# Kernel tuning notes

Hardware: AMD Instinct MI355X
Metric: run time of the kernel (lower is better)

The kernel has to match this reference:

```python
import jax, jax.numpy as jnp
import numpy as np

N0, N1, N2 = 100000, 25000, 5000
E0, E1 = 400000, 80000
IN_FEATS, N_HIDDEN, N_CLASSES = 512, 512, 64


def setup_inputs() -> dict:
    key = jax.random.key(0)
    ks = jax.random.split(key, 16)
    return {
        "feats": jax.random.normal(ks[0], (N0, IN_FEATS), jnp.float32),
        "h0_hist": jax.random.normal(ks[1], (N0, N_HIDDEN), jnp.float32),
        "agg_h0": jax.random.normal(ks[2], (N1, N_HIDDEN), jnp.float32),
        "h1_hist": jax.random.normal(ks[3], (N1, 2 * N_HIDDEN), jnp.float32),
        "agg_h1": jax.random.normal(ks[4], (N2, 2 * N_HIDDEN), jnp.float32),
        "W0": jax.random.normal(ks[5], (N_HIDDEN, IN_FEATS), jnp.float32) * 0.02,
        "b0": jax.random.normal(ks[6], (N_HIDDEN,), jnp.float32) * 0.02,
        "W1": jax.random.normal(ks[7], (N_HIDDEN, N_HIDDEN), jnp.float32) * 0.02,
        "b1": jax.random.normal(ks[8], (N_HIDDEN,), jnp.float32) * 0.02,
        "W2": jax.random.normal(ks[9], (N_CLASSES, 2 * N_HIDDEN), jnp.float32) * 0.02,
        "b2": jax.random.normal(ks[10], (N_CLASSES,), jnp.float32) * 0.02,
        "src0": jax.random.randint(ks[11], (E0,), 0, N0, jnp.int64),
        "dst0": jax.random.randint(ks[12], (E0,), 0, N1, jnp.int64),
        "src1": jax.random.randint(ks[13], (E1,), 0, N1, jnp.int64),
        "dst1": jax.random.randint(ks[14], (E1,), 0, N2, jnp.int64),
    }


def _segment_mean(h_src, src, dst, num_dst):
    # copy_src gather + variable-degree mean reduction (DGL fn.mean)
    msg = h_src[src]  # [E, D]
    sums = jax.ops.segment_sum(msg, dst, num_segments=num_dst)
    deg = jax.ops.segment_sum(jnp.ones((src.shape[0],), h_src.dtype), dst,
                              num_segments=num_dst)
    return sums / jnp.maximum(deg, 1.0)[:, None]


def reference(feats, h0_hist, agg_h0, h1_hist, agg_h1,
              W0, b0, W1, b1, W2, b2,
              src0, dst0, src1, dst1):
    # input layer: linear + relu (dropout=0)
    h = jax.nn.relu(feats @ W0.T + b0)  # [N0, H]

    # block 0: control-variate subtract, mean-aggregate, NodeUpdate(1) concat
    h = h - h0_hist
    agg = _segment_mean(h, src0, dst0, agg_h0.shape[0])  # [N1, H]
    h = (agg + agg_h0) @ W1.T + b1
    h = jnp.concatenate([h, jax.nn.relu(h)], axis=1)  # [N1, 2H]

    # block 1: control-variate subtract, mean-aggregate, NodeUpdate(2)
    h = h - h1_hist
    agg = _segment_mean(h, src1, dst1, agg_h1.shape[0])  # [N2, 2H]
    h = (agg + agg_h1) @ W2.T + b2  # [N2, C]
    return h
```

## Files before the change

kernel.cpp:

```cpp
#include <hip/hip_runtime.h>

#define N0c 100000
#define N1c 25000
#define N2c 5000
#define E0c 400000
#define E1c 80000

typedef __attribute__((ext_vector_type(8))) short bf16x8;
typedef __attribute__((ext_vector_type(4))) float f32x4;

#define GLOAD_LDS(g, l) \
    __builtin_amdgcn_global_load_lds((__attribute__((address_space(1))) const unsigned int*)(const void*)(g), \
                                     (__attribute__((address_space(3))) unsigned int*)(void*)(l), 16, 0, 0)

static __device__ __forceinline__ uint rnd_bf(float f) {
    uint u = __float_as_uint(f);
    return (u + 0x7FFFu + ((u >> 16) & 1u)) & 0xFFFF0000u;
}
static __device__ __forceinline__ unsigned short to_bf(float f) {
    return (unsigned short)(rnd_bf(f) >> 16);
}
static __device__ __forceinline__ uint pk_bf(float f0, float f1) {
    return (rnd_bf(f0) >> 16) | rnd_bf(f1);
}

__global__ __launch_bounds__(256)
void presplit_bf(const float* __restrict__ X, uint4* __restrict__ out,
                 int M, int tile0, int ntiles)
{
    const int id = blockIdx.x * 256 + threadIdx.x;
    const int slot = id & 1023;
    const int tk = id >> 10;
    if (tk >= ntiles * 8) return;
    const int kt8 = tk & 7, mtl = tk >> 3;
    const int r = slot >> 3, p = slot & 7;
    const int o = p ^ (r & 7);
    const int row = (tile0 + mtl) * 128 + r;
    uint4 v = {0u, 0u, 0u, 0u};
    if (row < M) {
        const float* src = X + (size_t)row * 512 + kt8 * 64 + o * 8;
        float4 x0 = *(const float4*)src;
        float4 x1 = *(const float4*)(src + 4);
        v.x = pk_bf(x0.x, x0.y); v.y = pk_bf(x0.z, x0.w);
        v.z = pk_bf(x1.x, x1.y); v.w = pk_bf(x1.z, x1.w);
    }
    out[(size_t)tk * 1024 + slot] = v;
}

template<int EPI>
__global__ __launch_bounds__(256, 2)
void gemm_bf16(const uint4* __restrict__ At, const uint4* __restrict__ Bt,
               const float* __restrict__ bias, const float* __restrict__ hist,
               unsigned short* __restrict__ C, int Mreal, int row_off, int nblk)
{
    __shared__ uint4 lds[2048];

    const int tid = threadIdx.x;
    const int orig = blockIdx.x;
    const int xcd = orig & 7, q = nblk >> 3, rr = nblk & 7;
    const int lid = (xcd < rr ? xcd * (q + 1) : rr * (q + 1) + (xcd - rr) * q) + (orig >> 3);
    const int bm = lid >> 2, bn = lid & 3;

    const int w = tid >> 6, lane = tid & 63;
    const int wm = w >> 1, wn = w & 1;
    const int lg = lane >> 4, lr = lane & 15;
    const int sw = lr & 7;
    const int sbase = w * 256;

    const uint4* Abase = At + (size_t)bm * 8 * 1024;
    const uint4* Bbase = Bt + (size_t)bn * 8 * 1024;

    f32x4 acc[4][4];
#pragma unroll
    for (int i = 0; i < 4; ++i)
#pragma unroll
        for (int j = 0; j < 4; ++j) acc[i][j] = {0.f, 0.f, 0.f, 0.f};

    for (int kt = 0; kt < 8; ++kt) {
        if (kt) __syncthreads();
        const uint4* Atile = Abase + (size_t)kt * 1024;
        const uint4* Btile = Bbase + (size_t)kt * 1024;
#pragma unroll
        for (int j = 0; j < 4; ++j) {
            const int slot = sbase + j * 64 + lane;
            GLOAD_LDS(Atile + slot, &lds[slot]);
            GLOAD_LDS(Btile + slot, &lds[1024 + slot]);
        }
        __syncthreads();

        bf16x8 a[4][2], b[4][2];
#pragma unroll
        for (int mi = 0; mi < 4; ++mi) {
            const uint4* rp = &lds[(wm * 64 + mi * 16 + lr) * 8];
            a[mi][0] = *(const bf16x8*)&rp[lg ^ sw];
            a[mi][1] = *(const bf16x8*)&rp[(4 + lg) ^ sw];
        }
#pragma unroll
        for (int ni = 0; ni < 4; ++ni) {
            const uint4* rp = &lds[1024 + (wn * 64 + ni * 16 + lr) * 8];
            b[ni][0] = *(const bf16x8*)&rp[lg ^ sw];
            b[ni][1] = *(const bf16x8*)&rp[(4 + lg) ^ sw];
        }
#pragma unroll
        for (int kk = 0; kk < 2; ++kk)
#pragma unroll
            for (int mi = 0; mi < 4; ++mi)
#pragma unroll
                for (int ni = 0; ni < 4; ++ni)
                    acc[mi][ni] = __builtin_amdgcn_mfma_f32_16x16x32_bf16(
                        a[mi][kk], b[ni][kk], acc[mi][ni], 0, 0, 0);
    }

#pragma unroll
    for (int mi = 0; mi < 4; ++mi)
#pragma unroll
        for (int ni = 0; ni < 4; ++ni) {
            const int col = bn * 128 + wn * 64 + ni * 16 + lr;
            const float bv = bias[col];
#pragma unroll
            for (int r = 0; r < 4; ++r) {
                const int m = row_off + bm * 128 + wm * 64 + mi * 16 + lg * 4 + r;
                if (m < Mreal) {
                    const float v = acc[mi][ni][r] + bv;
                    if (EPI == 0) {
                        C[(size_t)m * 512 + col] = to_bf(fmaxf(v, 0.f) - hist[(size_t)m * 512 + col]);
                    } else {
                        C[(size_t)m * 1024 + col]       = to_bf(v - hist[(size_t)m * 1024 + col]);
                        C[(size_t)m * 1024 + 512 + col] = to_bf(fmaxf(v, 0.f) - hist[(size_t)m * 1024 + 512 + col]);
                    }
                }
            }
        }
}

__global__ __launch_bounds__(256)
void gemm64(const float* __restrict__ A, const float* __restrict__ B,
            const float* __restrict__ bias, float* __restrict__ C, int M)
{
    const int K = 1024;
    __shared__ float As[32][68];
    __shared__ float Bs[32][68];
    const int tid = threadIdx.x;
    const int tx = tid & 15, ty = tid >> 4;
    const int lrow = tid >> 3;
    const int lk   = (tid & 7) * 4;
    const int bm = blockIdx.x;

    float acc[4][4];
#pragma unroll
    for (int i = 0; i < 4; ++i)
#pragma unroll
        for (int j = 0; j < 4; ++j) acc[i][j] = 0.f;

    int ar0 = bm * 64 + lrow;      if (ar0 > M - 1) ar0 = M - 1;
    int ar1 = bm * 64 + 32 + lrow; if (ar1 > M - 1) ar1 = M - 1;

    for (int kt = 0; kt < K; kt += 32) {
        float4 a0 = *(const float4*)(A + (size_t)ar0 * K + kt + lk);
        float4 a1 = *(const float4*)(A + (size_t)ar1 * K + kt + lk);
        float4 b0 = *(const float4*)(B + (size_t)lrow * K + kt + lk);
        float4 b1 = *(const float4*)(B + (size_t)(32 + lrow) * K + kt + lk);
        __syncthreads();
        As[lk+0][lrow]    = a0.x; As[lk+1][lrow]    = a0.y; As[lk+2][lrow]    = a0.z; As[lk+3][lrow]    = a0.w;
        As[lk+0][lrow+32] = a1.x; As[lk+1][lrow+32] = a1.y; As[lk+2][lrow+32] = a1.z; As[lk+3][lrow+32] = a1.w;
        Bs[lk+0][lrow]    = b0.x; Bs[lk+1][lrow]    = b0.y; Bs[lk+2][lrow]    = b0.z; Bs[lk+3][lrow]    = b0.w;
        Bs[lk+0][lrow+32] = b1.x; Bs[lk+1][lrow+32] = b1.y; Bs[lk+2][lrow+32] = b1.z; Bs[lk+3][lrow+32] = b1.w;
        __syncthreads();
#pragma unroll
        for (int kk = 0; kk < 32; ++kk) {
            float4 av = *(const float4*)&As[kk][ty * 4];
            float4 bv = *(const float4*)&Bs[kk][tx * 4];
            float aa[4] = {av.x, av.y, av.z, av.w};
            float bb[4] = {bv.x, bv.y, bv.z, bv.w};
#pragma unroll
            for (int i = 0; i < 4; ++i)
#pragma unroll
                for (int j = 0; j < 4; ++j)
                    acc[i][j] += aa[i] * bb[j];
        }
    }

    const float4 bv = *(const float4*)&bias[tx * 4];
#pragma unroll
    for (int i = 0; i < 4; ++i) {
        const int m = bm * 64 + ty * 4 + i;
        if (m >= M) continue;
        float4 o;
        o.x = acc[i][0] + bv.x; o.y = acc[i][1] + bv.y;
        o.z = acc[i][2] + bv.z; o.w = acc[i][3] + bv.w;
        *(float4*)&C[(size_t)m * 64 + tx * 4] = o;
    }
}

__global__ void count_deg(const int* __restrict__ dst, int* __restrict__ deg, int E)
{
    int e = blockIdx.x * blockDim.x + threadIdx.x;
    if (e < E) atomicAdd(&deg[dst[e]], 1);
}

__global__ __launch_bounds__(1024)
void exscan(const int* __restrict__ deg, int* __restrict__ off, int* __restrict__ cur, int n)
{
    __shared__ int wsum[16];
    __shared__ int carry;
    const int tid = threadIdx.x, lane = tid & 63, w = tid >> 6;
    if (tid == 0) carry = 0;
    __syncthreads();
    for (int base = 0; base < n; base += 1024) {
        const int i = base + tid;
        const int v = (i < n) ? deg[i] : 0;
        int x = v;
#pragma unroll
        for (int d = 1; d < 64; d <<= 1) {
            int y = __shfl_up(x, d, 64);
            if (lane >= d) x += y;
        }
        if (lane == 63) wsum[w] = x;
        __syncthreads();
        int wo = 0, tot = 0;
#pragma unroll
        for (int k = 0; k < 16; ++k) { int s = wsum[k]; tot += s; if (k < w) wo += s; }
        const int excl = carry + wo + x - v;
        if (i < n) { off[i] = excl; cur[i] = excl; }
        __syncthreads();
        if (tid == 0) carry += tot;
        __syncthreads();
    }
    if (tid == 0) off[n] = carry;
}

__global__ void scatter_edges(const int* __restrict__ src, const int* __restrict__ dst,
                              int* __restrict__ cur, int* __restrict__ eidx, int E)
{
    int e = blockIdx.x * blockDim.x + threadIdx.x;
    if (e < E) {
        int p = atomicAdd(&cur[dst[e]], 1);
        eidx[p] = src[e];
    }
}

__global__ __launch_bounds__(256)
void seg_mean_split(const unsigned short* __restrict__ h, const int* __restrict__ off,
                    const int* __restrict__ eidx, const float* __restrict__ addin,
                    uint4* __restrict__ out, int n_dst, int n_pad)
{
    const int wid = blockIdx.x * 4 + (threadIdx.x >> 6);
    const int lane = threadIdx.x & 63;
    if (wid >= n_pad) return;
    uint4 v = {0u, 0u, 0u, 0u};
    if (wid < n_dst) {
        const int e0 = off[wid], e1 = off[wid + 1];
        float s[8];
#pragma unroll
        for (int i = 0; i < 8; ++i) s[i] = 0.f;
        for (int e = e0; e < e1; ++e) {
            const uint4 vv = *((const uint4*)(h + (size_t)eidx[e] * 512) + lane);
            const uint u[4] = {vv.x, vv.y, vv.z, vv.w};
#pragma unroll
            for (int i = 0; i < 4; ++i) {
                s[2 * i]     += __uint_as_float(u[i] << 16);
                s[2 * i + 1] += __uint_as_float(u[i] & 0xFFFF0000u);
            }
        }
        const float sc = 1.0f / (float)((e1 - e0) > 0 ? (e1 - e0) : 1);
        const float* ad = addin + (size_t)wid * 512 + lane * 8;
        float4 d0 = *(const float4*)ad;
        float4 d1 = *(const float4*)(ad + 4);
        v.x = pk_bf(s[0] * sc + d0.x, s[1] * sc + d0.y);
        v.y = pk_bf(s[2] * sc + d0.z, s[3] * sc + d0.w);
        v.z = pk_bf(s[4] * sc + d1.x, s[5] * sc + d1.y);
        v.w = pk_bf(s[6] * sc + d1.z, s[7] * sc + d1.w);
    }
    const int mt = wid >> 7, r = wid & 127;
    const int kt8 = lane >> 3, o = lane & 7;
    out[((size_t)(mt * 8 + kt8)) * 1024 + r * 8 + (o ^ (r & 7))] = v;
}

__global__ __launch_bounds__(256)
void seg_mean_add4(const unsigned short* __restrict__ h, const int* __restrict__ off,
                   const int* __restrict__ eidx, const float* __restrict__ addin,
                   float* __restrict__ out, int n_dst)
{
    const int wid = blockIdx.x * 4 + (threadIdx.x >> 6);
    const int lane = threadIdx.x & 63;
    if (wid >= n_dst) return;
    const int e0 = off[wid], e1 = off[wid + 1];
    float s[16];
#pragma unroll
    for (int i = 0; i < 16; ++i) s[i] = 0.f;
    for (int e = e0; e < e1; ++e) {
        const uint4* row = (const uint4*)(h + (size_t)eidx[e] * 1024);
#pragma unroll
        for (int half = 0; half < 2; ++half) {
            const uint4 v = row[lane + 64 * half];
            const uint u[4] = {v.x, v.y, v.z, v.w};
#pragma unroll
            for (int i = 0; i < 4; ++i) {
                s[8 * half + 2 * i]     += __uint_as_float(u[i] << 16);
                s[8 * half + 2 * i + 1] += __uint_as_float(u[i] & 0xFFFF0000u);
            }
        }
    }
    const float sc = 1.0f / (float)((e1 - e0) > 0 ? (e1 - e0) : 1);
#pragma unroll
    for (int half = 0; half < 2; ++half) {
        const float* ad = addin + (size_t)wid * 1024 + half * 512 + lane * 8;
        float* o = out + (size_t)wid * 1024 + half * 512 + lane * 8;
        float4 d0 = *(const float4*)ad;
        float4 d1 = *(const float4*)(ad + 4);
        float4 r0, r1;
        r0.x = s[8*half+0] * sc + d0.x; r0.y = s[8*half+1] * sc + d0.y;
        r0.z = s[8*half+2] * sc + d0.z; r0.w = s[8*half+3] * sc + d0.w;
        r1.x = s[8*half+4] * sc + d1.x; r1.y = s[8*half+5] * sc + d1.y;
        r1.z = s[8*half+6] * sc + d1.z; r1.w = s[8*half+7] * sc + d1.w;
        *(float4*)o = r0;
        *(float4*)(o + 4) = r1;
    }
}

extern "C" void kernel_launch(void* const* d_in, const int* in_sizes, int n_in,
                              void* d_out, int out_size, void* d_ws, size_t ws_size,
                              hipStream_t stream)
{
    const float* feats   = (const float*)d_in[0];
    const float* h0_hist = (const float*)d_in[1];
    const float* agg_h0  = (const float*)d_in[2];
    const float* h1_hist = (const float*)d_in[3];
    const float* agg_h1  = (const float*)d_in[4];
    const float* W0 = (const float*)d_in[5];
    const float* b0 = (const float*)d_in[6];
    const float* W1 = (const float*)d_in[7];
    const float* b1 = (const float*)d_in[8];
    const float* W2 = (const float*)d_in[9];
    const float* b2 = (const float*)d_in[10];
    const int* src0 = (const int*)d_in[11];
    const int* dst0 = (const int*)d_in[12];
    const int* src1 = (const int*)d_in[13];
    const int* dst1 = (const int*)d_in[14];

    const int MT1 = 782;
    const int MT2 = 196;
    const size_t TILEB = 8 * 1024 * 16;

    const size_t h0B   = ((size_t)N0c * 512 * 2 + 255) & ~(size_t)255;
    const size_t a2B   = (size_t)MT2 * TILEB;
    const size_t agg1B = (size_t)N2c * 1024 * 4;
    const size_t wsB   = 4 * 8 * 1024 * 16;
    const size_t intB  = ((size_t)(N1c + (N1c + 1) + N1c + E0c + N2c + (N2c + 1) + N2c + E1c) * 4 + 255) & ~(size_t)255;
    const size_t FIXED = h0B + a2B + agg1B + 2 * wsB + intB;

    size_t avail = (ws_size > FIXED) ? (ws_size - FIXED) : 0;
    int ct = (int)(avail / TILEB);
    if (ct < 8) ct = 8;
    if (ct > MT1) ct = MT1;
    const int nchunks = (MT1 + ct - 1) / ct;

    char* ws = (char*)d_ws;
    uint4* Achunk = (uint4*)ws;                              ws += (size_t)ct * TILEB;
    unsigned short* h0 = (unsigned short*)ws;
    unsigned short* h1cat = h0;                              ws += h0B;
    uint4* A2s    = (uint4*)ws;                              ws += a2B;
    float* agg1   = (float*)ws;                              ws += agg1B;
    uint4* Ws0    = (uint4*)ws;                              ws += wsB;
    uint4* Ws1    = (uint4*)ws;                              ws += wsB;
    int* deg0  = (int*)ws;  ws += sizeof(int) * N1c;
    int* off0  = (int*)ws;  ws += sizeof(int) * (N1c + 1);
    int* cur0  = (int*)ws;  ws += sizeof(int) * N1c;
    int* eidx0 = (int*)ws;  ws += sizeof(int) * E0c;
    int* deg1  = (int*)ws;  ws += sizeof(int) * N2c;
    int* off1  = (int*)ws;  ws += sizeof(int) * (N2c + 1);
    int* cur1  = (int*)ws;  ws += sizeof(int) * N2c;
    int* eidx1 = (int*)ws;

    hipMemsetAsync(deg0, 0, sizeof(int) * N1c, stream);
    hipMemsetAsync(deg1, 0, sizeof(int) * N2c, stream);

    presplit_bf<<<4 * 32, 256, 0, stream>>>(W0, Ws0, 512, 0, 4);
    presplit_bf<<<4 * 32, 256, 0, stream>>>(W1, Ws1, 512, 0, 4);
    count_deg<<<(E0c + 255) / 256, 256, 0, stream>>>(dst0, deg0, E0c);
    exscan<<<1, 1024, 0, stream>>>(deg0, off0, cur0, N1c);
    scatter_edges<<<(E0c + 255) / 256, 256, 0, stream>>>(src0, dst0, cur0, eidx0, E0c);

    for (int c = 0; c < nchunks; ++c) {
        const int t0 = c * ct;
        const int nt = (MT1 - t0 < ct) ? (MT1 - t0) : ct;
        presplit_bf<<<nt * 32, 256, 0, stream>>>(feats, Achunk, N0c, t0, nt);
        const int nblk = nt * 4;
        gemm_bf16<0><<<nblk, 256, 0, stream>>>(Achunk, Ws0, b0, h0_hist, h0, N0c, t0 * 128, nblk);
    }

    seg_mean_split<<<(MT2 * 128) / 4, 256, 0, stream>>>(h0, off0, eidx0, agg_h0, A2s, N1c, MT2 * 128);

    count_deg<<<(E1c + 255) / 256, 256, 0, stream>>>(dst1, deg1, E1c);
    exscan<<<1, 1024, 0, stream>>>(deg1, off1, cur1, N2c);
    scatter_edges<<<(E1c + 255) / 256, 256, 0, stream>>>(src1, dst1, cur1, eidx1, E1c);

    gemm_bf16<1><<<MT2 * 4, 256, 0, stream>>>(A2s, Ws1, b1, h1_hist, h1cat, N1c, 0, MT2 * 4);

    seg_mean_add4<<<(N2c + 3) / 4, 256, 0, stream>>>(h1cat, off1, eidx1, agg_h1, agg1, N2c);

    gemm64<<<(N2c + 63) / 64, 256, 0, stream>>>(agg1, W2, b2, (float*)d_out, N2c);
}
```

Before: 592.1 us.

## Fuse fp32-to-bf16 conversion into a row-resident GEMM with double-buffered weights

Replaces the chunked presplit-then-GEMM flow with one kernel per layer. Each block keeps a full 128x512 A row-tile in LDS, converting fp32 feats to bf16 directly on load for layer 0, then loops over all four N tiles while double-buffering W slices. This removes the intermediate bf16 copy of feats (a large write plus re-read) and the repeated A loads across N tiles. In exchange it uses about 160KB of LDS for one block per CU, and the A tile load does not overlap with compute.

```diff
diff --git a/kernel.cpp b/kernel.cpp
--- a/kernel.cpp
+++ b/kernel.cpp
@@ -47,28 +47,56 @@
     out[(size_t)tk * 1024 + slot] = v;
 }
 
-template<int EPI>
-__global__ __launch_bounds__(256, 2)
-void gemm_bf16(const uint4* __restrict__ At, const uint4* __restrict__ Bt,
-               const float* __restrict__ bias, const float* __restrict__ hist,
-               unsigned short* __restrict__ C, int Mreal, int row_off, int nblk)
-{
-    __shared__ uint4 lds[2048];
+template<int SRC, int EPI>
+__global__ __launch_bounds__(256, 1)
+void gemm_persist(const float* __restrict__ Af32, const uint4* __restrict__ At,
+                  const uint4* __restrict__ Bt, const float* __restrict__ bias,
+                  const float* __restrict__ hist, unsigned short* __restrict__ C,
+                  int Mreal, int nblk)
+{
+    __shared__ uint4 lds[10240];
 
     const int tid = threadIdx.x;
     const int orig = blockIdx.x;
     const int xcd = orig & 7, q = nblk >> 3, rr = nblk & 7;
-    const int lid = (xcd < rr ? xcd * (q + 1) : rr * (q + 1) + (xcd - rr) * q) + (orig >> 3);
-    const int bm = lid >> 2, bn = lid & 3;
+    const int bm = (xcd < rr ? xcd * (q + 1) : rr * (q + 1) + (xcd - rr) * q) + (orig >> 3);
 
     const int w = tid >> 6, lane = tid & 63;
     const int wm = w >> 1, wn = w & 1;
     const int lg = lane >> 4, lr = lane & 15;
     const int sw = lr & 7;
-    const int sbase = w * 256;
-
-    const uint4* Abase = At + (size_t)bm * 8 * 1024;
-    const uint4* Bbase = Bt + (size_t)bn * 8 * 1024;
+
+    if (SRC == 0) {
+        const int r = tid >> 1, half = tid & 1;
+        int g = bm * 128 + r; if (g > Mreal - 1) g = Mreal - 1;
+        const float* Arow = Af32 + (size_t)g * 512 + half * 256;
+        const int abase = r * 8;
+        const int rsw = r & 7;
+#pragma unroll 8
+        for (int i = 0; i < 32; ++i) {
+            float4 x0 = *(const float4*)(Arow + i * 8);
+            float4 x1 = *(const float4*)(Arow + i * 8 + 4);
+            uint4 v;
+            v.x = pk_bf(x0.x, x0.y); v.y = pk_bf(x0.z, x0.w);
+            v.z = pk_bf(x1.x, x1.y); v.w = pk_bf(x1.z, x1.w);
+            const int kt = half * 4 + (i >> 3), o = i & 7;
+            lds[kt * 1024 + abase + (o ^ rsw)] = v;
+        }
+    } else {
+        const uint4* Ablk = At + (size_t)bm * 8192;
+#pragma unroll
+        for (int j = 0; j < 32; ++j) {
+            const int slot = w * 2048 + j * 64 + lane;
+            GLOAD_LDS(Ablk + slot, &lds[slot]);
+        }
+    }
+    {
+#pragma unroll
+        for (int j = 0; j < 4; ++j) {
+            const int slot = w * 256 + j * 64 + lane;
+            GLOAD_LDS(Bt + slot, &lds[8192 + slot]);
+        }
+    }
 
     f32x4 acc[4][4];
 #pragma unroll
@@ -76,30 +104,32 @@
 #pragma unroll
         for (int j = 0; j < 4; ++j) acc[i][j] = {0.f, 0.f, 0.f, 0.f};
 
-    for (int kt = 0; kt < 8; ++kt) {
-        if (kt) __syncthreads();
-        const uint4* Atile = Abase + (size_t)kt * 1024;
-        const uint4* Btile = Bbase + (size_t)kt * 1024;
-#pragma unroll
-        for (int j = 0; j < 4; ++j) {
-            const int slot = sbase + j * 64 + lane;
-            GLOAD_LDS(Atile + slot, &lds[slot]);
-            GLOAD_LDS(Btile + slot, &lds[1024 + slot]);
-        }
-        __syncthreads();
+    for (int s = 0; s < 32; ++s) {
+        __syncthreads();
+        if (s < 31) {
+            const uint4* Bn = Bt + (size_t)(s + 1) * 1024;
+            const int bb = 8192 + ((s + 1) & 1) * 1024;
+#pragma unroll
+            for (int j = 0; j < 4; ++j) {
+                const int slot = w * 256 + j * 64 + lane;
+                GLOAD_LDS(Bn + slot, &lds[bb + slot]);
+            }
+        }
+        const int kt = s & 7;
+        const int bbase = 8192 + (s & 1) * 1024;
 
         bf16x8 a[4][2], b[4][2];
 #pragma unroll
         for (int mi = 0; mi < 4; ++mi) {
-            const uint4* rp = &lds[(wm * 64 + mi * 16 + lr) * 8];
+            const uint4* rp = &lds[kt * 1024 + (wm * 64 + mi * 16 + lr) * 8];
             a[mi][0] = *(const bf16x8*)&rp[lg ^ sw];
             a[mi][1] = *(const bf16x8*)&rp[(4 + lg) ^ sw];
         }
 #pragma unroll
         for (int ni = 0; ni < 4; ++ni) {
-            const uint4* rp = &lds[1024 + (wn * 64 + ni * 16 + lr) * 8];
-            b[ni][0] = *(const bf16x8*)&rp[lg ^ sw];
-            b[ni][1] = *(const bf16x8*)&rp[(4 + lg) ^ sw];
+            const uint4* bp = &lds[bbase + (wn * 64 + ni * 16 + lr) * 8];
+            b[ni][0] = *(const bf16x8*)&bp[lg ^ sw];
+            b[ni][1] = *(const bf16x8*)&bp[(4 + lg) ^ sw];
         }
 #pragma unroll
         for (int kk = 0; kk < 2; ++kk)
@@ -109,28 +139,32 @@
                 for (int ni = 0; ni < 4; ++ni)
                     acc[mi][ni] = __builtin_amdgcn_mfma_f32_16x16x32_bf16(
                         a[mi][kk], b[ni][kk], acc[mi][ni], 0, 0, 0);
-    }
-
-#pragma unroll
-    for (int mi = 0; mi < 4; ++mi)
-#pragma unroll
-        for (int ni = 0; ni < 4; ++ni) {
-            const int col = bn * 128 + wn * 64 + ni * 16 + lr;
-            const float bv = bias[col];
-#pragma unroll
-            for (int r = 0; r < 4; ++r) {
-                const int m = row_off + bm * 128 + wm * 64 + mi * 16 + lg * 4 + r;
-                if (m < Mreal) {
-                    const float v = acc[mi][ni][r] + bv;
-                    if (EPI == 0) {
-                        C[(size_t)m * 512 + col] = to_bf(fmaxf(v, 0.f) - hist[(size_t)m * 512 + col]);
-                    } else {
-                        C[(size_t)m * 1024 + col]       = to_bf(v - hist[(size_t)m * 1024 + col]);
-                        C[(size_t)m * 1024 + 512 + col] = to_bf(fmaxf(v, 0.f) - hist[(size_t)m * 1024 + 512 + col]);
+
+        if ((s & 7) == 7) {
+            const int bn = s >> 3;
+#pragma unroll
+            for (int mi = 0; mi < 4; ++mi)
+#pragma unroll
+                for (int ni = 0; ni < 4; ++ni) {
+                    const int col = bn * 128 + wn * 64 + ni * 16 + lr;
+                    const float bv = bias[col];
+#pragma unroll
+                    for (int r = 0; r < 4; ++r) {
+                        const int m = bm * 128 + wm * 64 + mi * 16 + lg * 4 + r;
+                        if (m < Mreal) {
+                            const float v = acc[mi][ni][r] + bv;
+                            if (EPI == 0) {
+                                C[(size_t)m * 512 + col] = to_bf(fmaxf(v, 0.f) - hist[(size_t)m * 512 + col]);
+                            } else {
+                                C[(size_t)m * 1024 + col]       = to_bf(v - hist[(size_t)m * 1024 + col]);
+                                C[(size_t)m * 1024 + 512 + col] = to_bf(fmaxf(v, 0.f) - hist[(size_t)m * 1024 + 512 + col]);
+                            }
+                        }
+                        acc[mi][ni][r] = 0.f;
                     }
                 }
-            }
-        }
+        }
+    }
 }
 
 __global__ __launch_bounds__(256)
@@ -346,17 +380,8 @@
     const size_t a2B   = (size_t)MT2 * TILEB;
     const size_t agg1B = (size_t)N2c * 1024 * 4;
     const size_t wsB   = 4 * 8 * 1024 * 16;
-    const size_t intB  = ((size_t)(N1c + (N1c + 1) + N1c + E0c + N2c + (N2c + 1) + N2c + E1c) * 4 + 255) & ~(size_t)255;
-    const size_t FIXED = h0B + a2B + agg1B + 2 * wsB + intB;
-
-    size_t avail = (ws_size > FIXED) ? (ws_size - FIXED) : 0;
-    int ct = (int)(avail / TILEB);
-    if (ct < 8) ct = 8;
-    if (ct > MT1) ct = MT1;
-    const int nchunks = (MT1 + ct - 1) / ct;
 
     char* ws = (char*)d_ws;
-    uint4* Achunk = (uint4*)ws;                              ws += (size_t)ct * TILEB;
     unsigned short* h0 = (unsigned short*)ws;
     unsigned short* h1cat = h0;                              ws += h0B;
     uint4* A2s    = (uint4*)ws;                              ws += a2B;
@@ -381,13 +406,7 @@
     exscan<<<1, 1024, 0, stream>>>(deg0, off0, cur0, N1c);
     scatter_edges<<<(E0c + 255) / 256, 256, 0, stream>>>(src0, dst0, cur0, eidx0, E0c);
 
-    for (int c = 0; c < nchunks; ++c) {
-        const int t0 = c * ct;
-        const int nt = (MT1 - t0 < ct) ? (MT1 - t0) : ct;
-        presplit_bf<<<nt * 32, 256, 0, stream>>>(feats, Achunk, N0c, t0, nt);
-        const int nblk = nt * 4;
-        gemm_bf16<0><<<nblk, 256, 0, stream>>>(Achunk, Ws0, b0, h0_hist, h0, N0c, t0 * 128, nblk);
-    }
+    gemm_persist<0, 0><<<MT1, 256, 0, stream>>>(feats, nullptr, Ws0, b0, h0_hist, h0, N0c, MT1);
 
     seg_mean_split<<<(MT2 * 128) / 4, 256, 0, stream>>>(h0, off0, eidx0, agg_h0, A2s, N1c, MT2 * 128);
 
@@ -395,7 +414,7 @@
     exscan<<<1, 1024, 0, stream>>>(deg1, off1, cur1, N2c);
     scatter_edges<<<(E1c + 255) / 256, 256, 0, stream>>>(src1, dst1, cur1, eidx1, E1c);
 
-    gemm_bf16<1><<<MT2 * 4, 256, 0, stream>>>(A2s, Ws1, b1, h1_hist, h1cat, N1c, 0, MT2 * 4);
+    gemm_persist<1, 1><<<MT2, 256, 0, stream>>>(nullptr, A2s, Ws1, b1, h1_hist, h1cat, N1c, MT2);
 
     seg_mean_add4<<<(N2c + 3) / 4, 256, 0, stream>>>(h1cat, off1, eidx1, agg_h1, agg1, N2c);
 
```

New measurement: 917.4 us. +54.9%, slower.

## Fuse fp32-to-bf16 conversion into first GEMM and widen tiles to 128x256

Applied to the files above, without the earlier changes.

The first layer GEMM now reads fp32 feats directly, converts them to bf16 and stores them into swizzled LDS, so the separate presplit pass and the chunked workspace round-trip are gone. Both bf16 GEMMs move to 512-thread blocks computing 128x256 output tiles, which halves how often each A tile is re-read across N-blocks. The cost is synchronous register-staged A loads in the first GEMM instead of async global-to-LDS copies, plus a larger LDS footprint and more threads per block.

```diff
diff --git a/kernel.cpp b/kernel.cpp
--- a/kernel.cpp
+++ b/kernel.cpp
@@ -47,28 +47,28 @@
     out[(size_t)tk * 1024 + slot] = v;
 }
 
-template<int EPI>
-__global__ __launch_bounds__(256, 2)
-void gemm_bf16(const uint4* __restrict__ At, const uint4* __restrict__ Bt,
-               const float* __restrict__ bias, const float* __restrict__ hist,
-               unsigned short* __restrict__ C, int Mreal, int row_off, int nblk)
-{
-    __shared__ uint4 lds[2048];
+template<int SRC, int EPI>
+__global__ __launch_bounds__(512, 2)
+void gemm_half(const float* __restrict__ Af32, const uint4* __restrict__ At,
+               const uint4* __restrict__ Bt, const float* __restrict__ bias,
+               const float* __restrict__ hist, unsigned short* __restrict__ C,
+               int Mreal, int nblk)
+{
+    __shared__ uint4 lds[3072];
 
     const int tid = threadIdx.x;
     const int orig = blockIdx.x;
     const int xcd = orig & 7, q = nblk >> 3, rr = nblk & 7;
     const int lid = (xcd < rr ? xcd * (q + 1) : rr * (q + 1) + (xcd - rr) * q) + (orig >> 3);
-    const int bm = lid >> 2, bn = lid & 3;
+    const int bm = lid >> 1, bnh = lid & 1;
 
     const int w = tid >> 6, lane = tid & 63;
-    const int wm = w >> 1, wn = w & 1;
+    const int wm = w >> 2, wn = w & 3;
     const int lg = lane >> 4, lr = lane & 15;
-    const int sw = lr & 7;
-    const int sbase = w * 256;
-
-    const uint4* Abase = At + (size_t)bm * 8 * 1024;
-    const uint4* Bbase = Bt + (size_t)bn * 8 * 1024;
+    const int sw = lr & 15 & 7;
+
+    const int ar = tid >> 3;
+    const int as = tid & 7;
 
     f32x4 acc[4][4];
 #pragma unroll
@@ -78,13 +78,32 @@
 
     for (int kt = 0; kt < 8; ++kt) {
         if (kt) __syncthreads();
-        const uint4* Atile = Abase + (size_t)kt * 1024;
-        const uint4* Btile = Bbase + (size_t)kt * 1024;
+        if (SRC == 0) {
+#pragma unroll
+            for (int u = 0; u < 2; ++u) {
+                const int r = ar + u * 64;
+                const int o = as ^ (r & 7);
+                int g = bm * 128 + r; if (g > Mreal - 1) g = Mreal - 1;
+                const float* p = Af32 + (size_t)g * 512 + kt * 64 + o * 8;
+                float4 x0 = *(const float4*)p;
+                float4 x1 = *(const float4*)(p + 4);
+                uint4 v;
+                v.x = pk_bf(x0.x, x0.y); v.y = pk_bf(x0.z, x0.w);
+                v.z = pk_bf(x1.x, x1.y); v.w = pk_bf(x1.z, x1.w);
+                lds[r * 8 + as] = v;
+            }
+        } else {
+            const uint4* Ablk = At + ((size_t)bm * 8 + kt) * 1024;
+            GLOAD_LDS(Ablk + tid, &lds[tid]);
+            GLOAD_LDS(Ablk + 512 + tid, &lds[512 + tid]);
+        }
 #pragma unroll
         for (int j = 0; j < 4; ++j) {
-            const int slot = sbase + j * 64 + lane;
-            GLOAD_LDS(Atile + slot, &lds[slot]);
-            GLOAD_LDS(Btile + slot, &lds[1024 + slot]);
+            const int sl = w * 256 + j * 64 + lane;
+            const int sub = sl >> 10;
+            const int off = sl & 1023;
+            GLOAD_LDS(Bt + ((size_t)(2 * bnh + sub) * 8 + kt) * 1024 + off,
+                      &lds[1024 + sl]);
         }
         __syncthreads();
 
@@ -115,11 +134,11 @@
     for (int mi = 0; mi < 4; ++mi)
 #pragma unroll
         for (int ni = 0; ni < 4; ++ni) {
-            const int col = bn * 128 + wn * 64 + ni * 16 + lr;
+            const int col = bnh * 256 + wn * 64 + ni * 16 + lr;
             const float bv = bias[col];
 #pragma unroll
             for (int r = 0; r < 4; ++r) {
-                const int m = row_off + bm * 128 + wm * 64 + mi * 16 + lg * 4 + r;
+                const int m = bm * 128 + wm * 64 + mi * 16 + lg * 4 + r;
                 if (m < Mreal) {
                     const float v = acc[mi][ni][r] + bv;
                     if (EPI == 0) {
@@ -346,17 +365,8 @@
     const size_t a2B   = (size_t)MT2 * TILEB;
     const size_t agg1B = (size_t)N2c * 1024 * 4;
     const size_t wsB   = 4 * 8 * 1024 * 16;
-    const size_t intB  = ((size_t)(N1c + (N1c + 1) + N1c + E0c + N2c + (N2c + 1) + N2c + E1c) * 4 + 255) & ~(size_t)255;
-    const size_t FIXED = h0B + a2B + agg1B + 2 * wsB + intB;
-
-    size_t avail = (ws_size > FIXED) ? (ws_size - FIXED) : 0;
-    int ct = (int)(avail / TILEB);
-    if (ct < 8) ct = 8;
-    if (ct > MT1) ct = MT1;
-    const int nchunks = (MT1 + ct - 1) / ct;
 
     char* ws = (char*)d_ws;
-    uint4* Achunk = (uint4*)ws;                              ws += (size_t)ct * TILEB;
     unsigned short* h0 = (unsigned short*)ws;
     unsigned short* h1cat = h0;                              ws += h0B;
     uint4* A2s    = (uint4*)ws;                              ws += a2B;
@@ -381,13 +391,7 @@
     exscan<<<1, 1024, 0, stream>>>(deg0, off0, cur0, N1c);
     scatter_edges<<<(E0c + 255) / 256, 256, 0, stream>>>(src0, dst0, cur0, eidx0, E0c);
 
-    for (int c = 0; c < nchunks; ++c) {
-        const int t0 = c * ct;
-        const int nt = (MT1 - t0 < ct) ? (MT1 - t0) : ct;
-        presplit_bf<<<nt * 32, 256, 0, stream>>>(feats, Achunk, N0c, t0, nt);
-        const int nblk = nt * 4;
-        gemm_bf16<0><<<nblk, 256, 0, stream>>>(Achunk, Ws0, b0, h0_hist, h0, N0c, t0 * 128, nblk);
-    }
+    gemm_half<0, 0><<<MT1 * 2, 512, 0, stream>>>(feats, nullptr, Ws0, b0, h0_hist, h0, N0c, MT1 * 2);
 
     seg_mean_split<<<(MT2 * 128) / 4, 256, 0, stream>>>(h0, off0, eidx0, agg_h0, A2s, N1c, MT2 * 128);
 
@@ -395,7 +399,7 @@
     exscan<<<1, 1024, 0, stream>>>(deg1, off1, cur1, N2c);
     scatter_edges<<<(E1c + 255) / 256, 256, 0, stream>>>(src1, dst1, cur1, eidx1, E1c);
 
-    gemm_bf16<1><<<MT2 * 4, 256, 0, stream>>>(A2s, Ws1, b1, h1_hist, h1cat, N1c, 0, MT2 * 4);
+    gemm_half<1, 1><<<MT2 * 2, 512, 0, stream>>>(nullptr, A2s, Ws1, b1, h1_hist, h1cat, N1c, MT2 * 2);
 
     seg_mean_add4<<<(N2c + 3) / 4, 256, 0, stream>>>(h1cat, off1, eidx1, agg_h1, agg1, N2c);
 
```

After: 639.0 us. 7.9% more time.
